# Kernel optimization log

Measured on AMD Instinct MI355X. Metric: run time of the kernel, lower is better.

Reference implementation:

```python
import jax, jax.numpy as jnp
import numpy as np
import math

B, T, N, FIN, C, E = 32, 10, 1000, 1, 96, 8000
NEG_SLOPE = 0.2


def _sinusoidal_pos_embed(stepsize, embedding_size):
    position = jnp.arange(stepsize, dtype=jnp.float32)[:, None]
    div_term = jnp.exp(jnp.arange(0, embedding_size, 2, dtype=jnp.float32)
                       * (-math.log(10000.0) / embedding_size))
    pe = jnp.zeros((stepsize, embedding_size), dtype=jnp.float32)
    pe = pe.at[:, 0::2].set(jnp.sin(position * div_term))
    pe = pe.at[:, 1::2].set(jnp.cos(position * div_term))
    return pe  # [T, C]


def setup_inputs() -> dict:
    key = jax.random.key(0)
    k_x, k_s, k_d, k_wl, k_wr, k_a = jax.random.split(key, 6)
    x = jax.random.normal(k_x, (B, T, N, FIN), dtype=jnp.float32)
    src = jax.random.randint(k_s, (E,), 0, N)
    dst = jax.random.randint(k_d, (E,), 0, N)
    edge_index = jnp.stack([src, dst]).astype(jnp.int32)
    s_in = 1.0 / np.sqrt(FIN)
    Wl = jax.random.uniform(k_wl, (FIN, C), jnp.float32, -s_in, s_in)
    Wr = jax.random.uniform(k_wr, (FIN, C), jnp.float32, -s_in, s_in)
    bl = jnp.zeros((C,), jnp.float32)
    br = jnp.zeros((C,), jnp.float32)
    s_a = 1.0 / np.sqrt(C)
    att = jax.random.uniform(k_a, (C,), jnp.float32, -s_a, s_a)
    bias = jnp.zeros((C,), jnp.float32)
    return dict(x=x, edge_index=edge_index, Wl=Wl, bl=bl, Wr=Wr, br=br,
                att=att, bias=bias)


def reference(x, edge_index, Wl, bl, Wr, br, att, bias):
    Bb, Tt, Nn, Fin = x.shape
    Cc = Wl.shape[1]
    # GATv2Conv default add_self_loops=True
    loops = jnp.arange(Nn, dtype=edge_index.dtype)
    src = jnp.concatenate([edge_index[0], loops])  # message sources j
    dst = jnp.concatenate([edge_index[1], loops])  # message targets i

    xg = x.reshape(Bb * Tt, Nn, Fin)                 # [G, N, Fin]
    xl = xg @ Wl + bl                                # lin_l(x_j)  [G, N, C]
    xr = xg @ Wr + br                                # lin_r(x_i)  [G, N, C]

    # GATv2 attention logits: a^T LeakyReLU(xl[j] + xr[i])
    e = jax.nn.leaky_relu(xl[:, src] + xr[:, dst], NEG_SLOPE) @ att  # [G, Etot]

    def per_graph(e_g, xl_g):
        m = jax.ops.segment_max(e_g, dst, num_segments=Nn)
        ex = jnp.exp(e_g - m[dst])
        denom = jax.ops.segment_sum(ex, dst, num_segments=Nn)
        alpha = ex / denom[dst]                       # softmax over incoming edges
        msgs = alpha[:, None] * xl_g[src]             # [Etot, C]
        return jax.ops.segment_sum(msgs, dst, num_segments=Nn)  # [N, C]

    out = jax.vmap(per_graph)(e, xl) + bias           # [G, N, C]
    out = out.reshape(Bb, Tt, Nn, Cc)

    pos = _sinusoidal_pos_embed(Tt, Cc)               # [T, C]
    out = out + pos[None, :, None, :]
    return out.reshape(Bb, Tt * Nn, Cc)
```

## Files before the change

kernel.cpp:

```cpp
#include <hip/hip_runtime.h>
#include <math.h>

#define G_ 320
#define N_ 1000
#define T_ 10
#define C_ 96
#define E_ 8000
#define QN 250
#define CAP 2816
#define EPT 5


__global__ __launch_bounds__(512) void kA(
        const int* __restrict__ ei,
        const float* __restrict__ Wl, const float* __restrict__ bl,
        const float* __restrict__ Wr, const float* __restrict__ br,
        const float* __restrict__ att,
        float4* __restrict__ P, float* __restrict__ lin3g,
        int* __restrict__ offsG, int2* __restrict__ slots) {
    __shared__ int cnt[256], cur[256], offsL[260];
    const int tid = threadIdx.x;
    const int q = blockIdx.x;
    const int lo = q * QN;

    if (q == 0) {
        if (tid < C_)
            P[tid] = make_float4(Wl[tid], Wr[tid], bl[tid] + br[tid], 0.4f * att[tid]);
        int w = tid >> 6, lane = tid & 63;
        if (w < 3) {
            float s = 0.f;
            for (int i = lane; i < C_; i += 64) {
                float a = att[i];
                float m = (w == 0) ? Wl[i] : (w == 1) ? Wr[i] : (bl[i] + br[i]);
                s += a * m;
            }
            for (int off = 32; off; off >>= 1) s += __shfl_down(s, off);
            if (lane == 0) lin3g[w] = 0.6f * s;
        }
    }
    for (int i = tid; i < 256; i += 512) cnt[i] = (i < QN) ? 1 : 0;
    __syncthreads();

    const int4* d4 = (const int4*)(ei + E_);
    const int4* s4 = (const int4*)ei;
    for (int j = tid; j < E_ / 4; j += 512) {
        int4 d = d4[j];
        int r0 = d.x - lo, r1 = d.y - lo, r2 = d.z - lo, r3 = d.w - lo;
        if ((unsigned)r0 < (unsigned)QN) atomicAdd(&cnt[r0], 1);
        if ((unsigned)r1 < (unsigned)QN) atomicAdd(&cnt[r1], 1);
        if ((unsigned)r2 < (unsigned)QN) atomicAdd(&cnt[r2], 1);
        if ((unsigned)r3 < (unsigned)QN) atomicAdd(&cnt[r3], 1);
    }
    __syncthreads();

    if (tid < 64) {
        int b4 = tid * 4;
        int a0 = cnt[b4], a1 = cnt[b4 + 1], a2 = cnt[b4 + 2], a3 = cnt[b4 + 3];
        int s1 = a0 + a1, s2 = s1 + a2, s3 = s2 + a3;
        int pre = s3;
        for (int off = 1; off < 64; off <<= 1) {
            int tv = __shfl_up(pre, off);
            if (tid >= off) pre += tv;
        }
        int base = pre - s3;
        offsL[b4] = base;          cur[b4] = base;
        offsL[b4 + 1] = base + a0; cur[b4 + 1] = base + a0;
        offsL[b4 + 2] = base + s1; cur[b4 + 2] = base + s1;
        offsL[b4 + 3] = base + s2; cur[b4 + 3] = base + s2;
    }
    __syncthreads();

    int2* sl = slots + (size_t)q * CAP;
    for (int j = tid; j < E_ / 4; j += 512) {
        int4 d = d4[j];
        int4 s = s4[j];
#define SCAT(DD, SS) { int r = (DD) - lo;                                    \
        if ((unsigned)r < (unsigned)QN) {                                    \
            int pos = atomicAdd(&cur[r], 1);                                 \
            sl[pos] = make_int2((SS), (DD)); } }
        SCAT(d.x, s.x) SCAT(d.y, s.y) SCAT(d.z, s.z) SCAT(d.w, s.w)
#undef SCAT
    }
    for (int i = tid; i < QN; i += 512) {
        int pos = atomicAdd(&cur[i], 1);
        sl[pos] = make_int2(lo + i, lo + i);
    }
    for (int i = tid; i <= QN; i += 512) offsG[q * (QN + 1) + i] = offsL[i];
}

__global__ __launch_bounds__(512, 4) void kF(
        const float* __restrict__ x, const float4* __restrict__ P,
        const float* __restrict__ lin3g, const int* __restrict__ offsG,
        const int2* __restrict__ slots,
        const float* __restrict__ Wl, const float* __restrict__ bl,
        const float* __restrict__ bias, float4* __restrict__ out) {
    __shared__ float xgs[N_];
    __shared__ float L[CAP];
    __shared__ float U[CAP];
    __shared__ int offsL[QN + 1];
    __shared__ float Sloc[QN];
    __shared__ float4 wl4[C_ / 4], cb4[C_ / 4];
    const int tid = threadIdx.x;
    const int q = blockIdx.x;
    const int g = blockIdx.y;
    const int lo = q * QN;
    const int t = g % T_;

    const float* xg = x + g * N_;
    if (tid < N_ / 4) ((float4*)xgs)[tid] = ((const float4*)xg)[tid];
    for (int i = tid; i <= QN; i += 512) offsL[i] = offsG[q * (QN + 1) + i];
    if (tid < C_) {
        int k2 = tid & ~1;
        float dt = __expf(-(float)k2 * (logf(10000.0f) / (float)C_));
        float ang = (float)t * dt;
        float pe = (tid & 1) ? cosf(ang) : sinf(ang);
        ((float*)wl4)[tid] = Wl[tid];
        ((float*)cb4)[tid] = bl[tid] + bias[tid] + pe;
    }
    __syncthreads();
    const int cntE = offsL[QN];
    const float la = lin3g[0], lb = lin3g[1], lc = lin3g[2];
    const int2* sl = slots + (size_t)q * CAP;

    {
        float u[EPT], v[EPT], acc[EPT];
#pragma unroll
        for (int k = 0; k < EPT; k++) {
            int p = tid + k * 512;
            int2 sd = sl[p < cntE ? p : 0];
            u[k] = xgs[sd.x]; v[k] = xgs[sd.y]; acc[k] = 0.f;
        }
#pragma unroll 8
        for (int c = 0; c < C_; c++) {
            float4 qv = P[c];
#pragma unroll
            for (int k = 0; k < EPT; k++) {
                float wv = fmaf(u[k], qv.x, fmaf(v[k], qv.y, qv.z));
                acc[k] = fmaf(qv.w, fabsf(wv), acc[k]);
            }
        }
#pragma unroll
        for (int k = 0; k < EPT; k++) {
            int p = tid + k * 512;
            if (p < cntE) {
                L[p] = fmaf(u[k], la, fmaf(v[k], lb, lc)) + acc[k];
                U[p] = u[k];
            }
        }
    }
    for (int p = tid + 512 * EPT; p < cntE; p += 512) {
        int2 sd = sl[p];
        float uu = xgs[sd.x], vv = xgs[sd.y], a2 = 0.f;
        for (int c = 0; c < C_; c++) {
            float4 qv = P[c];
            float wv = fmaf(uu, qv.x, fmaf(vv, qv.y, qv.z));
            a2 = fmaf(qv.w, fabsf(wv), a2);
        }
        L[p] = fmaf(uu, la, fmaf(vv, lb, lc)) + a2;
        U[p] = uu;
    }
    __syncthreads();

    if (tid < QN) {
        int a = offsL[tid], b = offsL[tid + 1];
        float m = -INFINITY, den = 0.f, num = 0.f;
        for (int p = a; p < b; ++p) {
            float l = L[p], uu = U[p];
            float nm = fmaxf(m, l);
            float sc = __expf(m - nm);
            float ex = __expf(l - nm);
            den = den * sc + ex;
            num = fmaf(ex, uu, num * sc);
            m = nm;
        }
        Sloc[tid] = num / den;
    }
    __syncthreads();

    float4* out4 = out + (size_t)(g * N_ + lo) * (C_ / 4);
    int node = tid / 24, c4 = tid % 24;
    for (int i = tid; i < QN * (C_ / 4); i += 512) {
        float s = Sloc[node];
        float4 wv = wl4[c4], cb = cb4[c4];
        out4[i] = make_float4(fmaf(s, wv.x, cb.x), fmaf(s, wv.y, cb.y),
                              fmaf(s, wv.z, cb.z), fmaf(s, wv.w, cb.w));
        int c4n = c4 + 8;
        int carry = (c4n >= 24) ? 1 : 0;
        node += 21 + carry;
        c4 = c4n - (carry ? 24 : 0);
    }
}

extern "C" void kernel_launch(void* const* d_in, const int* in_sizes, int n_in,
                              void* d_out, int out_size, void* d_ws, size_t ws_size,
                              hipStream_t stream) {
    const float* x    = (const float*)d_in[0];
    const int*   ei   = (const int*)d_in[1];
    const float* Wl   = (const float*)d_in[2];
    const float* bl   = (const float*)d_in[3];
    const float* Wr   = (const float*)d_in[4];
    const float* br   = (const float*)d_in[5];
    const float* att  = (const float*)d_in[6];
    const float* bias = (const float*)d_in[7];
    float4* out = (float4*)d_out;

    char* ws = (char*)d_ws;
    float4* P     = (float4*)(ws + 0);
    float*  lin3g = (float*)(ws + 1536);
    int*    offsG = (int*)(ws + 1552);
    int2*   slots = (int2*)(ws + 5568);

    hipLaunchKernelGGL(kA, dim3(4), dim3(512), 0, stream,
                       ei, Wl, bl, Wr, br, att, P, lin3g, offsG, slots);
    hipLaunchKernelGGL(kF, dim3(4, G_), dim3(512), 0, stream,
                       x, P, lin3g, offsG, slots, Wl, bl, bias, out);
}
```

Measured before the change: 52.06 us.

## Split work into per-wavefront node slices processed in chunks without block barriers

Graph nodes are split into 8 slices of 125 instead of 4 of 250, and each 64-lane wavefront of a 128-thread block owns one slice. Each wavefront walks its slice in chunks of 16 nodes, computing edge logits, the softmax aggregation and the output writes per chunk without block-wide barriers. This lets logit compute, softmax and stores from different wavefronts interleave and shrinks shared memory per block. In exchange it adds per-chunk serial phases, a fixed CCAP edge buffer that could overflow on dense chunks, and uneven work across wavefronts.

```diff
diff --git a/kernel.cpp b/kernel.cpp
--- a/kernel.cpp
+++ b/kernel.cpp
@@ -6,9 +6,12 @@
 #define T_ 10
 #define C_ 96
 #define E_ 8000
-#define QN 250
-#define CAP 2816
-#define EPT 5
+#define NSLICE 8
+#define NS 125
+#define CAP2 1500
+#define CCAP 320
+#define CHN 16
+#define NCH 8
 
 
 __global__ __launch_bounds__(512) void kA(
@@ -18,10 +21,10 @@
         const float* __restrict__ att,
         float4* __restrict__ P, float* __restrict__ lin3g,
         int* __restrict__ offsG, int2* __restrict__ slots) {
-    __shared__ int cnt[256], cur[256], offsL[260];
+    __shared__ int cnt[128], cur[128], offsL[130];
     const int tid = threadIdx.x;
     const int q = blockIdx.x;
-    const int lo = q * QN;
+    const int lo = q * NS;
 
     if (q == 0) {
         if (tid < C_)
@@ -38,7 +41,7 @@
             if (lane == 0) lin3g[w] = 0.6f * s;
         }
     }
-    for (int i = tid; i < 256; i += 512) cnt[i] = (i < QN) ? 1 : 0;
+    for (int i = tid; i < 128; i += 512) cnt[i] = (i < NS) ? 1 : 0;
     __syncthreads();
 
     const int4* d4 = (const int4*)(ei + E_);
@@ -46,148 +49,143 @@
     for (int j = tid; j < E_ / 4; j += 512) {
         int4 d = d4[j];
         int r0 = d.x - lo, r1 = d.y - lo, r2 = d.z - lo, r3 = d.w - lo;
-        if ((unsigned)r0 < (unsigned)QN) atomicAdd(&cnt[r0], 1);
-        if ((unsigned)r1 < (unsigned)QN) atomicAdd(&cnt[r1], 1);
-        if ((unsigned)r2 < (unsigned)QN) atomicAdd(&cnt[r2], 1);
-        if ((unsigned)r3 < (unsigned)QN) atomicAdd(&cnt[r3], 1);
+        if ((unsigned)r0 < (unsigned)NS) atomicAdd(&cnt[r0], 1);
+        if ((unsigned)r1 < (unsigned)NS) atomicAdd(&cnt[r1], 1);
+        if ((unsigned)r2 < (unsigned)NS) atomicAdd(&cnt[r2], 1);
+        if ((unsigned)r3 < (unsigned)NS) atomicAdd(&cnt[r3], 1);
     }
     __syncthreads();
 
     if (tid < 64) {
-        int b4 = tid * 4;
-        int a0 = cnt[b4], a1 = cnt[b4 + 1], a2 = cnt[b4 + 2], a3 = cnt[b4 + 3];
-        int s1 = a0 + a1, s2 = s1 + a2, s3 = s2 + a3;
-        int pre = s3;
+        int b2 = tid * 2;
+        int a0 = cnt[b2], a1 = cnt[b2 + 1];
+        int s = a0 + a1;
+        int pre = s;
         for (int off = 1; off < 64; off <<= 1) {
             int tv = __shfl_up(pre, off);
             if (tid >= off) pre += tv;
         }
-        int base = pre - s3;
-        offsL[b4] = base;          cur[b4] = base;
-        offsL[b4 + 1] = base + a0; cur[b4 + 1] = base + a0;
-        offsL[b4 + 2] = base + s1; cur[b4 + 2] = base + s1;
-        offsL[b4 + 3] = base + s2; cur[b4 + 3] = base + s2;
-    }
-    __syncthreads();
-
-    int2* sl = slots + (size_t)q * CAP;
+        int base = pre - s;
+        offsL[b2] = base;          cur[b2] = base;
+        offsL[b2 + 1] = base + a0; cur[b2 + 1] = base + a0;
+    }
+    __syncthreads();
+
+    int2* sl = slots + (size_t)q * CAP2;
     for (int j = tid; j < E_ / 4; j += 512) {
         int4 d = d4[j];
         int4 s = s4[j];
 #define SCAT(DD, SS) { int r = (DD) - lo;                                    \
-        if ((unsigned)r < (unsigned)QN) {                                    \
+        if ((unsigned)r < (unsigned)NS) {                                    \
             int pos = atomicAdd(&cur[r], 1);                                 \
             sl[pos] = make_int2((SS), (DD)); } }
         SCAT(d.x, s.x) SCAT(d.y, s.y) SCAT(d.z, s.z) SCAT(d.w, s.w)
 #undef SCAT
     }
-    for (int i = tid; i < QN; i += 512) {
+    for (int i = tid; i < NS; i += 512) {
         int pos = atomicAdd(&cur[i], 1);
         sl[pos] = make_int2(lo + i, lo + i);
     }
-    for (int i = tid; i <= QN; i += 512) offsG[q * (QN + 1) + i] = offsL[i];
+    for (int i = tid; i <= NS; i += 512) offsG[q * (NS + 1) + i] = offsL[i];
 }
 
-__global__ __launch_bounds__(512, 4) void kF(
+__global__ __launch_bounds__(128, 4) void kF(
         const float* __restrict__ x, const float4* __restrict__ P,
         const float* __restrict__ lin3g, const int* __restrict__ offsG,
         const int2* __restrict__ slots,
         const float* __restrict__ Wl, const float* __restrict__ bl,
         const float* __restrict__ bias, float4* __restrict__ out) {
     __shared__ float xgs[N_];
-    __shared__ float L[CAP];
-    __shared__ float U[CAP];
-    __shared__ int offsL[QN + 1];
-    __shared__ float Sloc[QN];
-    __shared__ float4 wl4[C_ / 4], cb4[C_ / 4];
+    __shared__ float Lb[2][CCAP];
+    __shared__ float Ub[2][CCAP];
+    __shared__ int offsW[2][NS + 1];
+    __shared__ float Sch[2][CHN];
+    __shared__ float4 wl4s[C_ / 4], cb4s[C_ / 4];
+
     const int tid = threadIdx.x;
-    const int q = blockIdx.x;
-    const int g = blockIdx.y;
-    const int lo = q * QN;
+    const int w = tid >> 6, lane = tid & 63;
+    const int qh = blockIdx.x, g = blockIdx.y;
+    const int slice = qh * 2 + w;
+    const int lo = slice * NS;
     const int t = g % T_;
 
     const float* xg = x + g * N_;
-    if (tid < N_ / 4) ((float4*)xgs)[tid] = ((const float4*)xg)[tid];
-    for (int i = tid; i <= QN; i += 512) offsL[i] = offsG[q * (QN + 1) + i];
+    for (int i = tid; i < N_ / 4; i += 128)
+        ((float4*)xgs)[i] = ((const float4*)xg)[i];
     if (tid < C_) {
         int k2 = tid & ~1;
         float dt = __expf(-(float)k2 * (logf(10000.0f) / (float)C_));
         float ang = (float)t * dt;
         float pe = (tid & 1) ? cosf(ang) : sinf(ang);
-        ((float*)wl4)[tid] = Wl[tid];
-        ((float*)cb4)[tid] = bl[tid] + bias[tid] + pe;
-    }
-    __syncthreads();
-    const int cntE = offsL[QN];
+        ((float*)wl4s)[tid] = Wl[tid];
+        ((float*)cb4s)[tid] = bl[tid] + bias[tid] + pe;
+    }
+    for (int i = lane; i <= NS; i += 64)
+        offsW[w][i] = offsG[slice * (NS + 1) + i];
+    __syncthreads();
+
     const float la = lin3g[0], lb = lin3g[1], lc = lin3g[2];
-    const int2* sl = slots + (size_t)q * CAP;
-
-    {
-        float u[EPT], v[EPT], acc[EPT];
-#pragma unroll
-        for (int k = 0; k < EPT; k++) {
-            int p = tid + k * 512;
-            int2 sd = sl[p < cntE ? p : 0];
-            u[k] = xgs[sd.x]; v[k] = xgs[sd.y]; acc[k] = 0.f;
-        }
+    const int2* sl = slots + (size_t)slice * CAP2;
+
+    for (int ch = 0; ch < NCH; ++ch) {
+        const int n0 = ch * CHN;
+        const int nch = (NS - n0 < CHN) ? (NS - n0) : CHN;
+        const int s0 = offsW[w][n0];
+        const int s1 = offsW[w][n0 + nch];
+
+        for (int p = s0 + lane; p < s1; p += 128) {
+            int p1 = p + 64;
+            bool ok1 = p1 < s1;
+            int2 sd0 = sl[p];
+            int2 sd1 = sl[ok1 ? p1 : p];
+            float u0 = xgs[sd0.x], v0 = xgs[sd0.y];
+            float u1 = xgs[sd1.x], v1 = xgs[sd1.y];
+            float a0 = 0.f, a1 = 0.f;
 #pragma unroll 8
-        for (int c = 0; c < C_; c++) {
-            float4 qv = P[c];
-#pragma unroll
-            for (int k = 0; k < EPT; k++) {
-                float wv = fmaf(u[k], qv.x, fmaf(v[k], qv.y, qv.z));
-                acc[k] = fmaf(qv.w, fabsf(wv), acc[k]);
-            }
-        }
-#pragma unroll
-        for (int k = 0; k < EPT; k++) {
-            int p = tid + k * 512;
-            if (p < cntE) {
-                L[p] = fmaf(u[k], la, fmaf(v[k], lb, lc)) + acc[k];
-                U[p] = u[k];
-            }
-        }
-    }
-    for (int p = tid + 512 * EPT; p < cntE; p += 512) {
-        int2 sd = sl[p];
-        float uu = xgs[sd.x], vv = xgs[sd.y], a2 = 0.f;
-        for (int c = 0; c < C_; c++) {
-            float4 qv = P[c];
-            float wv = fmaf(uu, qv.x, fmaf(vv, qv.y, qv.z));
-            a2 = fmaf(qv.w, fabsf(wv), a2);
-        }
-        L[p] = fmaf(uu, la, fmaf(vv, lb, lc)) + a2;
-        U[p] = uu;
-    }
-    __syncthreads();
-
-    if (tid < QN) {
-        int a = offsL[tid], b = offsL[tid + 1];
-        float m = -INFINITY, den = 0.f, num = 0.f;
-        for (int p = a; p < b; ++p) {
-            float l = L[p], uu = U[p];
-            float nm = fmaxf(m, l);
-            float sc = __expf(m - nm);
-            float ex = __expf(l - nm);
-            den = den * sc + ex;
-            num = fmaf(ex, uu, num * sc);
-            m = nm;
-        }
-        Sloc[tid] = num / den;
-    }
-    __syncthreads();
-
-    float4* out4 = out + (size_t)(g * N_ + lo) * (C_ / 4);
-    int node = tid / 24, c4 = tid % 24;
-    for (int i = tid; i < QN * (C_ / 4); i += 512) {
-        float s = Sloc[node];
-        float4 wv = wl4[c4], cb = cb4[c4];
-        out4[i] = make_float4(fmaf(s, wv.x, cb.x), fmaf(s, wv.y, cb.y),
-                              fmaf(s, wv.z, cb.z), fmaf(s, wv.w, cb.w));
-        int c4n = c4 + 8;
-        int carry = (c4n >= 24) ? 1 : 0;
-        node += 21 + carry;
-        c4 = c4n - (carry ? 24 : 0);
+            for (int c = 0; c < C_; c++) {
+                float4 qv = P[c];
+                float w0 = fmaf(u0, qv.x, fmaf(v0, qv.y, qv.z));
+                float w1 = fmaf(u1, qv.x, fmaf(v1, qv.y, qv.z));
+                a0 = fmaf(qv.w, fabsf(w0), a0);
+                a1 = fmaf(qv.w, fabsf(w1), a1);
+            }
+            Lb[w][p - s0] = fmaf(u0, la, fmaf(v0, lb, lc)) + a0;
+            Ub[w][p - s0] = u0;
+            if (ok1) {
+                Lb[w][p1 - s0] = fmaf(u1, la, fmaf(v1, lb, lc)) + a1;
+                Ub[w][p1 - s0] = u1;
+            }
+        }
+
+        if (lane < nch) {
+            int a = offsW[w][n0 + lane] - s0;
+            int b = offsW[w][n0 + lane + 1] - s0;
+            float m = -INFINITY, den = 0.f, num = 0.f;
+            for (int p = a; p < b; ++p) {
+                float l = Lb[w][p], uu = Ub[w][p];
+                float nm = fmaxf(m, l);
+                float sc = __expf(m - nm);
+                float ex = __expf(l - nm);
+                den = den * sc + ex;
+                num = fmaf(ex, uu, num * sc);
+                m = nm;
+            }
+            Sch[w][lane] = num / den;
+        }
+
+        float4* out4 = out + (size_t)(g * N_ + lo + n0) * (C_ / 4);
+        const int tot = nch * (C_ / 4);
+        int node = lane / 24, c4 = lane % 24;
+        for (int i = lane; i < tot; i += 64) {
+            float s = Sch[w][node];
+            float4 wv = wl4s[c4], cb = cb4s[c4];
+            out4[i] = make_float4(fmaf(s, wv.x, cb.x), fmaf(s, wv.y, cb.y),
+                                  fmaf(s, wv.z, cb.z), fmaf(s, wv.w, cb.w));
+            int c4n = c4 + 16;
+            int carry = (c4n >= 24) ? 1 : 0;
+            node += 2 + carry;
+            c4 = c4n - (carry ? 24 : 0);
+        }
     }
 }
 
@@ -208,10 +206,10 @@
     float4* P     = (float4*)(ws + 0);
     float*  lin3g = (float*)(ws + 1536);
     int*    offsG = (int*)(ws + 1552);
-    int2*   slots = (int2*)(ws + 5568);
-
-    hipLaunchKernelGGL(kA, dim3(4), dim3(512), 0, stream,
+    int2*   slots = (int2*)(ws + 5584);
+
+    hipLaunchKernelGGL(kA, dim3(NSLICE), dim3(512), 0, stream,
                        ei, Wl, bl, Wr, br, att, P, lin3g, offsG, slots);
-    hipLaunchKernelGGL(kF, dim3(4, G_), dim3(512), 0, stream,
+    hipLaunchKernelGGL(kF, dim3(NSLICE / 2, G_), dim3(128), 0, stream,
                        x, P, lin3g, offsG, slots, Wl, bl, bias, out);
 }
```

Measured after the change: 91.25 us. 75.3% more time.

## Process two graphs per block and overlap output writes with next logits

Applied to the files above, without the earlier changes.

Each block of the main kernel now handles two consecutive graphs, halving the grid. The output store of the first graph is issued without a barrier before the second graph's logit computation, so global writes can overlap with compute. Logit and source value arrays are packed into one float2 array. This amortizes block setup (offset loads, positional-embedding constants) but halves the number of blocks, which may reduce parallelism and latency hiding.

```diff
diff --git a/kernel.cpp b/kernel.cpp
--- a/kernel.cpp
+++ b/kernel.cpp
@@ -88,47 +88,53 @@
     for (int i = tid; i <= QN; i += 512) offsG[q * (QN + 1) + i] = offsL[i];
 }
 
-__global__ __launch_bounds__(512, 4) void kF(
+__global__ __launch_bounds__(512, 4) void kF2(
         const float* __restrict__ x, const float4* __restrict__ P,
         const float* __restrict__ lin3g, const int* __restrict__ offsG,
         const int2* __restrict__ slots,
         const float* __restrict__ Wl, const float* __restrict__ bl,
         const float* __restrict__ bias, float4* __restrict__ out) {
-    __shared__ float xgs[N_];
-    __shared__ float L[CAP];
-    __shared__ float U[CAP];
+    __shared__ float xgs[2][N_];
+    __shared__ float2 LU[CAP];
     __shared__ int offsL[QN + 1];
-    __shared__ float Sloc[QN];
-    __shared__ float4 wl4[C_ / 4], cb4[C_ / 4];
+    __shared__ float Sloc[2][QN];
+    __shared__ float4 wl4[C_ / 4];
+    __shared__ float4 cb4[2][C_ / 4];
+
     const int tid = threadIdx.x;
     const int q = blockIdx.x;
-    const int g = blockIdx.y;
+    const int g0 = blockIdx.y * 2;
     const int lo = q * QN;
-    const int t = g % T_;
-
-    const float* xg = x + g * N_;
-    if (tid < N_ / 4) ((float4*)xgs)[tid] = ((const float4*)xg)[tid];
+
+    const float4* xg4 = (const float4*)(x + (size_t)g0 * N_);
+    for (int i = tid; i < 2 * N_ / 4; i += 512) ((float4*)xgs)[i] = xg4[i];
     for (int i = tid; i <= QN; i += 512) offsL[i] = offsG[q * (QN + 1) + i];
-    if (tid < C_) {
-        int k2 = tid & ~1;
+    if (tid < 2 * C_) {
+        int it = tid / C_, c = tid % C_;
+        int t = (g0 + it) % T_;
+        int k2 = c & ~1;
         float dt = __expf(-(float)k2 * (logf(10000.0f) / (float)C_));
         float ang = (float)t * dt;
-        float pe = (tid & 1) ? cosf(ang) : sinf(ang);
-        ((float*)wl4)[tid] = Wl[tid];
-        ((float*)cb4)[tid] = bl[tid] + bias[tid] + pe;
-    }
-    __syncthreads();
+        float pe = (c & 1) ? cosf(ang) : sinf(ang);
+        ((float*)cb4[it])[c] = bl[c] + bias[c] + pe;
+    } else if (tid < 3 * C_) {
+        int c = tid - 2 * C_;
+        ((float*)wl4)[c] = Wl[c];
+    }
+    __syncthreads();
+
     const int cntE = offsL[QN];
     const float la = lin3g[0], lb = lin3g[1], lc = lin3g[2];
     const int2* sl = slots + (size_t)q * CAP;
 
-    {
+    auto logits = [&](int it) {
+        const float* xx = xgs[it];
         float u[EPT], v[EPT], acc[EPT];
 #pragma unroll
         for (int k = 0; k < EPT; k++) {
             int p = tid + k * 512;
             int2 sd = sl[p < cntE ? p : 0];
-            u[k] = xgs[sd.x]; v[k] = xgs[sd.y]; acc[k] = 0.f;
+            u[k] = xx[sd.x]; v[k] = xx[sd.y]; acc[k] = 0.f;
         }
 #pragma unroll 8
         for (int c = 0; c < C_; c++) {
@@ -142,53 +148,63 @@
 #pragma unroll
         for (int k = 0; k < EPT; k++) {
             int p = tid + k * 512;
-            if (p < cntE) {
-                L[p] = fmaf(u[k], la, fmaf(v[k], lb, lc)) + acc[k];
-                U[p] = u[k];
-            }
-        }
-    }
-    for (int p = tid + 512 * EPT; p < cntE; p += 512) {
-        int2 sd = sl[p];
-        float uu = xgs[sd.x], vv = xgs[sd.y], a2 = 0.f;
-        for (int c = 0; c < C_; c++) {
-            float4 qv = P[c];
-            float wv = fmaf(uu, qv.x, fmaf(vv, qv.y, qv.z));
-            a2 = fmaf(qv.w, fabsf(wv), a2);
-        }
-        L[p] = fmaf(uu, la, fmaf(vv, lb, lc)) + a2;
-        U[p] = uu;
-    }
-    __syncthreads();
-
-    if (tid < QN) {
-        int a = offsL[tid], b = offsL[tid + 1];
-        float m = -INFINITY, den = 0.f, num = 0.f;
-        for (int p = a; p < b; ++p) {
-            float l = L[p], uu = U[p];
-            float nm = fmaxf(m, l);
-            float sc = __expf(m - nm);
-            float ex = __expf(l - nm);
-            den = den * sc + ex;
-            num = fmaf(ex, uu, num * sc);
-            m = nm;
-        }
-        Sloc[tid] = num / den;
-    }
-    __syncthreads();
-
-    float4* out4 = out + (size_t)(g * N_ + lo) * (C_ / 4);
-    int node = tid / 24, c4 = tid % 24;
-    for (int i = tid; i < QN * (C_ / 4); i += 512) {
-        float s = Sloc[node];
-        float4 wv = wl4[c4], cb = cb4[c4];
-        out4[i] = make_float4(fmaf(s, wv.x, cb.x), fmaf(s, wv.y, cb.y),
-                              fmaf(s, wv.z, cb.z), fmaf(s, wv.w, cb.w));
-        int c4n = c4 + 8;
-        int carry = (c4n >= 24) ? 1 : 0;
-        node += 21 + carry;
-        c4 = c4n - (carry ? 24 : 0);
-    }
+            if (p < cntE)
+                LU[p] = make_float2(fmaf(u[k], la, fmaf(v[k], lb, lc)) + acc[k], u[k]);
+        }
+        for (int p = tid + 512 * EPT; p < cntE; p += 512) {
+            int2 sd = sl[p];
+            float uu = xx[sd.x], vv = xx[sd.y], a2 = 0.f;
+            for (int c = 0; c < C_; c++) {
+                float4 qv = P[c];
+                float wv = fmaf(uu, qv.x, fmaf(vv, qv.y, qv.z));
+                a2 = fmaf(qv.w, fabsf(wv), a2);
+            }
+            LU[p] = make_float2(fmaf(uu, la, fmaf(vv, lb, lc)) + a2, uu);
+        }
+    };
+
+    auto softmax = [&](int it) {
+        if (tid < QN) {
+            int a = offsL[tid], b = offsL[tid + 1];
+            float m = -INFINITY, den = 0.f, num = 0.f;
+            for (int p = a; p < b; ++p) {
+                float2 lu = LU[p];
+                float nm = fmaxf(m, lu.x);
+                float sc = __expf(m - nm);
+                float ex = __expf(lu.x - nm);
+                den = den * sc + ex;
+                num = fmaf(ex, lu.y, num * sc);
+                m = nm;
+            }
+            Sloc[it][tid] = num / den;
+        }
+    };
+
+    auto writeout = [&](int it) {
+        float4* out4 = out + (size_t)((g0 + it) * N_ + lo) * (C_ / 4);
+        int node = tid / 24, c4 = tid % 24;
+        for (int i = tid; i < QN * (C_ / 4); i += 512) {
+            float s = Sloc[it][node];
+            float4 wv = wl4[c4], cb = cb4[it][c4];
+            out4[i] = make_float4(fmaf(s, wv.x, cb.x), fmaf(s, wv.y, cb.y),
+                                  fmaf(s, wv.z, cb.z), fmaf(s, wv.w, cb.w));
+            int c4n = c4 + 8;
+            int carry = (c4n >= 24) ? 1 : 0;
+            node += 21 + carry;
+            c4 = c4n - (carry ? 24 : 0);
+        }
+    };
+
+    logits(0);
+    __syncthreads();
+    softmax(0);
+    __syncthreads();
+    writeout(0);
+    logits(1);
+    __syncthreads();
+    softmax(1);
+    __syncthreads();
+    writeout(1);
 }
 
 extern "C" void kernel_launch(void* const* d_in, const int* in_sizes, int n_in,
@@ -212,6 +228,6 @@
 
     hipLaunchKernelGGL(kA, dim3(4), dim3(512), 0, stream,
                        ei, Wl, bl, Wr, br, att, P, lin3g, offsG, slots);
-    hipLaunchKernelGGL(kF, dim3(4, G_), dim3(512), 0, stream,
+    hipLaunchKernelGGL(kF2, dim3(4, G_ / 2), dim3(512), 0, stream,
                        x, P, lin3g, offsG, slots, Wl, bl, bias, out);
 }
```

After: 57.51 us. 10.5% more time.

## Fuse CSR build into main kernel and tabulate attention logits via homogeneity

Applied to the files above, without the earlier changes.

Merges the CSR-building kernel and the main kernel into one launch. Each block now rebuilds its own dst-bucketed edge list in shared memory, with indices packed into 16-bit halves, so global slot buffers and the second launch go away. When the combined lin_l/lin_r bias is zero, the 96-channel LeakyReLU-attention sum per edge is replaced by a piecewise-linear table lookup. This relies on the sum being homogeneous in (x_j, x_i), which turns the per-edge C-loop into a few ops. The costs are redundant per-block table and CSR construction, interpolation error from a 129-point table, and smaller blocks of 256 threads.

```diff
diff --git a/kernel.cpp b/kernel.cpp
--- a/kernel.cpp
+++ b/kernel.cpp
@@ -8,24 +8,39 @@
 #define E_ 8000
 #define QN 250
 #define CAP 2816
-#define EPT 5
-
-
-__global__ __launch_bounds__(512) void kA(
-        const int* __restrict__ ei,
+#define NTB 129
+
+__global__ __launch_bounds__(256, 6) void kAll(
+        const float* __restrict__ x, const int* __restrict__ ei,
         const float* __restrict__ Wl, const float* __restrict__ bl,
         const float* __restrict__ Wr, const float* __restrict__ br,
-        const float* __restrict__ att,
-        float4* __restrict__ P, float* __restrict__ lin3g,
-        int* __restrict__ offsG, int2* __restrict__ slots) {
-    __shared__ int cnt[256], cur[256], offsL[260];
+        const float* __restrict__ att, const float* __restrict__ bias,
+        float4* __restrict__ out) {
+    __shared__ float xgs[N_];
+    __shared__ int   slots[CAP];
+    __shared__ int   cnt[256], cur[256], offsL[260];
+    __shared__ float tabL[2 * NTB];
+    __shared__ float Sloc[QN];
+    __shared__ float4 wl4[C_ / 4], cb4[C_ / 4];
+    __shared__ float lin4[4];
+
     const int tid = threadIdx.x;
-    const int q = blockIdx.x;
+    const int q = blockIdx.x, g = blockIdx.y;
     const int lo = q * QN;
-
-    if (q == 0) {
-        if (tid < C_)
-            P[tid] = make_float4(Wl[tid], Wr[tid], bl[tid] + br[tid], 0.4f * att[tid]);
+    const int t = g % T_;
+
+    if (tid < N_ / 4)
+        ((float4*)xgs)[tid] = ((const float4*)(x + (size_t)g * N_))[tid];
+    cnt[tid] = (tid < QN) ? 1 : 0;
+    if (tid < C_) {
+        int k2 = tid & ~1;
+        float dt = __expf(-(float)k2 * (logf(10000.0f) / (float)C_));
+        float ang = (float)t * dt;
+        float pe = (tid & 1) ? cosf(ang) : sinf(ang);
+        ((float*)wl4)[tid] = Wl[tid];
+        ((float*)cb4)[tid] = bl[tid] + bias[tid] + pe;
+    }
+    {
         int w = tid >> 6, lane = tid & 63;
         if (w < 3) {
             float s = 0.f;
@@ -35,15 +50,31 @@
                 s += a * m;
             }
             for (int off = 32; off; off >>= 1) s += __shfl_down(s, off);
-            if (lane == 0) lin3g[w] = 0.6f * s;
-        }
-    }
-    for (int i = tid; i < 256; i += 512) cnt[i] = (i < QN) ? 1 : 0;
+            if (lane == 0) lin4[w] = 0.6f * s;
+        } else {
+            float m = 0.f;
+            for (int i = lane; i < C_; i += 64) m = fmaxf(m, fabsf(bl[i] + br[i]));
+            for (int off = 32; off; off >>= 1) m = fmaxf(m, __shfl_down(m, off));
+            if (lane == 0) lin4[3] = (m == 0.f) ? 1.f : 0.f;
+        }
+    }
+    for (int i = tid; i < 2 * NTB; i += 256) {
+        int which = (i >= NTB);
+        int j = i - which * NTB;
+        float tt = -1.f + (float)j * (2.f / (float)(NTB - 1));
+        float s = 0.f;
+        for (int c = 0; c < C_; c++) {
+            float wl = Wl[c], wr = Wr[c];
+            float val = which ? fmaf(tt, wl, wr) : fmaf(tt, wr, wl);
+            s = fmaf(0.4f * att[c], fabsf(val), s);
+        }
+        tabL[i] = s;
+    }
     __syncthreads();
 
     const int4* d4 = (const int4*)(ei + E_);
     const int4* s4 = (const int4*)ei;
-    for (int j = tid; j < E_ / 4; j += 512) {
+    for (int j = tid; j < E_ / 4; j += 256) {
         int4 d = d4[j];
         int r0 = d.x - lo, r1 = d.y - lo, r2 = d.z - lo, r3 = d.w - lo;
         if ((unsigned)r0 < (unsigned)QN) atomicAdd(&cnt[r0], 1);
@@ -70,108 +101,68 @@
     }
     __syncthreads();
 
-    int2* sl = slots + (size_t)q * CAP;
-    for (int j = tid; j < E_ / 4; j += 512) {
+    for (int j = tid; j < E_ / 4; j += 256) {
         int4 d = d4[j];
         int4 s = s4[j];
 #define SCAT(DD, SS) { int r = (DD) - lo;                                    \
         if ((unsigned)r < (unsigned)QN) {                                    \
             int pos = atomicAdd(&cur[r], 1);                                 \
-            sl[pos] = make_int2((SS), (DD)); } }
+            slots[pos] = (SS) | ((DD) << 16); } }
         SCAT(d.x, s.x) SCAT(d.y, s.y) SCAT(d.z, s.z) SCAT(d.w, s.w)
 #undef SCAT
     }
-    for (int i = tid; i < QN; i += 512) {
-        int pos = atomicAdd(&cur[i], 1);
-        sl[pos] = make_int2(lo + i, lo + i);
-    }
-    for (int i = tid; i <= QN; i += 512) offsG[q * (QN + 1) + i] = offsL[i];
-}
-
-__global__ __launch_bounds__(512, 4) void kF(
-        const float* __restrict__ x, const float4* __restrict__ P,
-        const float* __restrict__ lin3g, const int* __restrict__ offsG,
-        const int2* __restrict__ slots,
-        const float* __restrict__ Wl, const float* __restrict__ bl,
-        const float* __restrict__ bias, float4* __restrict__ out) {
-    __shared__ float xgs[N_];
-    __shared__ float L[CAP];
-    __shared__ float U[CAP];
-    __shared__ int offsL[QN + 1];
-    __shared__ float Sloc[QN];
-    __shared__ float4 wl4[C_ / 4], cb4[C_ / 4];
-    const int tid = threadIdx.x;
-    const int q = blockIdx.x;
-    const int g = blockIdx.y;
-    const int lo = q * QN;
-    const int t = g % T_;
-
-    const float* xg = x + g * N_;
-    if (tid < N_ / 4) ((float4*)xgs)[tid] = ((const float4*)xg)[tid];
-    for (int i = tid; i <= QN; i += 512) offsL[i] = offsG[q * (QN + 1) + i];
-    if (tid < C_) {
-        int k2 = tid & ~1;
-        float dt = __expf(-(float)k2 * (logf(10000.0f) / (float)C_));
-        float ang = (float)t * dt;
-        float pe = (tid & 1) ? cosf(ang) : sinf(ang);
-        ((float*)wl4)[tid] = Wl[tid];
-        ((float*)cb4)[tid] = bl[tid] + bias[tid] + pe;
-    }
-    __syncthreads();
-    const int cntE = offsL[QN];
-    const float la = lin3g[0], lb = lin3g[1], lc = lin3g[2];
-    const int2* sl = slots + (size_t)q * CAP;
-
-    {
-        float u[EPT], v[EPT], acc[EPT];
-#pragma unroll
-        for (int k = 0; k < EPT; k++) {
-            int p = tid + k * 512;
-            int2 sd = sl[p < cntE ? p : 0];
-            u[k] = xgs[sd.x]; v[k] = xgs[sd.y]; acc[k] = 0.f;
-        }
-#pragma unroll 8
-        for (int c = 0; c < C_; c++) {
-            float4 qv = P[c];
-#pragma unroll
-            for (int k = 0; k < EPT; k++) {
-                float wv = fmaf(u[k], qv.x, fmaf(v[k], qv.y, qv.z));
-                acc[k] = fmaf(qv.w, fabsf(wv), acc[k]);
-            }
-        }
-#pragma unroll
-        for (int k = 0; k < EPT; k++) {
-            int p = tid + k * 512;
-            if (p < cntE) {
-                L[p] = fmaf(u[k], la, fmaf(v[k], lb, lc)) + acc[k];
-                U[p] = u[k];
-            }
-        }
-    }
-    for (int p = tid + 512 * EPT; p < cntE; p += 512) {
-        int2 sd = sl[p];
-        float uu = xgs[sd.x], vv = xgs[sd.y], a2 = 0.f;
-        for (int c = 0; c < C_; c++) {
-            float4 qv = P[c];
-            float wv = fmaf(uu, qv.x, fmaf(vv, qv.y, qv.z));
-            a2 = fmaf(qv.w, fabsf(wv), a2);
-        }
-        L[p] = fmaf(uu, la, fmaf(vv, lb, lc)) + a2;
-        U[p] = uu;
-    }
-    __syncthreads();
-
+    if (tid < QN) {
+        int nid = lo + tid;
+        int pos = atomicAdd(&cur[tid], 1);
+        slots[pos] = nid | (nid << 16);
+    }
+    __syncthreads();
+
+    const float la = lin4[0], lb = lin4[1], lc = lin4[2];
+    const bool homog = (lin4[3] != 0.f);
     if (tid < QN) {
         int a = offsL[tid], b = offsL[tid + 1];
         float m = -INFINITY, den = 0.f, num = 0.f;
-        for (int p = a; p < b; ++p) {
-            float l = L[p], uu = U[p];
-            float nm = fmaxf(m, l);
-            float sc = __expf(m - nm);
-            float ex = __expf(l - nm);
-            den = den * sc + ex;
-            num = fmaf(ex, uu, num * sc);
-            m = nm;
+        if (homog) {
+            for (int p = a; p < b; ++p) {
+                int sd = slots[p];
+                float uu = xgs[sd & 0xFFFF], vv = xgs[sd >> 16];
+                float au = fabsf(uu), av = fabsf(vv);
+                bool ub = au >= av;
+                float big = ub ? au : av;
+                float tt = (ub ? vv : uu) / (ub ? uu : vv);
+                tt = fmaxf(fminf(tt, 1.f), -1.f);
+                float fi = fmaf(tt, 64.f, 64.f);
+                int i0 = (int)fi; i0 = min(i0, NTB - 2);
+                float fr = fi - (float)i0;
+                int bse = ub ? 0 : NTB;
+                float t0 = tabL[bse + i0], t1 = tabL[bse + i0 + 1];
+                float l = fmaf(big, fmaf(fr, t1 - t0, t0),
+                               fmaf(uu, la, fmaf(vv, lb, lc)));
+                float nm = fmaxf(m, l);
+                float sc = __expf(m - nm);
+                float ex = __expf(l - nm);
+                den = den * sc + ex;
+                num = fmaf(ex, uu, num * sc);
+                m = nm;
+            }
+        } else {
+            for (int p = a; p < b; ++p) {
+                int sd = slots[p];
+                float uu = xgs[sd & 0xFFFF], vv = xgs[sd >> 16];
+                float a2 = 0.f;
+                for (int c = 0; c < C_; c++) {
+                    float wv = fmaf(uu, Wl[c], fmaf(vv, Wr[c], bl[c] + br[c]));
+                    a2 = fmaf(0.4f * att[c], fabsf(wv), a2);
+                }
+                float l = fmaf(uu, la, fmaf(vv, lb, lc)) + a2;
+                float nm = fmaxf(m, l);
+                float sc = __expf(m - nm);
+                float ex = __expf(l - nm);
+                den = den * sc + ex;
+                num = fmaf(ex, uu, num * sc);
+                m = nm;
+            }
         }
         Sloc[tid] = num / den;
     }
@@ -179,14 +170,14 @@
 
     float4* out4 = out + (size_t)(g * N_ + lo) * (C_ / 4);
     int node = tid / 24, c4 = tid % 24;
-    for (int i = tid; i < QN * (C_ / 4); i += 512) {
+    for (int i = tid; i < QN * (C_ / 4); i += 256) {
         float s = Sloc[node];
         float4 wv = wl4[c4], cb = cb4[c4];
         out4[i] = make_float4(fmaf(s, wv.x, cb.x), fmaf(s, wv.y, cb.y),
                               fmaf(s, wv.z, cb.z), fmaf(s, wv.w, cb.w));
-        int c4n = c4 + 8;
+        int c4n = c4 + 16;
         int carry = (c4n >= 24) ? 1 : 0;
-        node += 21 + carry;
+        node += 10 + carry;
         c4 = c4n - (carry ? 24 : 0);
     }
 }
@@ -204,14 +195,6 @@
     const float* bias = (const float*)d_in[7];
     float4* out = (float4*)d_out;
 
-    char* ws = (char*)d_ws;
-    float4* P     = (float4*)(ws + 0);
-    float*  lin3g = (float*)(ws + 1536);
-    int*    offsG = (int*)(ws + 1552);
-    int2*   slots = (int2*)(ws + 5568);
-
-    hipLaunchKernelGGL(kA, dim3(4), dim3(512), 0, stream,
-                       ei, Wl, bl, Wr, br, att, P, lin3g, offsG, slots);
-    hipLaunchKernelGGL(kF, dim3(4, G_), dim3(512), 0, stream,
-                       x, P, lin3g, offsG, slots, Wl, bl, bias, out);
+    hipLaunchKernelGGL(kAll, dim3(4, G_), dim3(256), 0, stream,
+                       x, ei, Wl, bl, Wr, br, att, bias, out);
 }
```

Measured after the change: 42.44 us (median of 2 runs). -18.5%, faster.
